# Kernel tuning notes

Hardware: AMD Instinct MI355X
Metric: run time of the kernel (lower is better)

The kernel has to match this reference:

```python
import jax, jax.numpy as jnp
import numpy as np

GROUPS = [21, 6, 17, 14, 20]
N = 78          # total nodes per graph
B = 8192        # batched graphs (original module processes one at a time)
RATIO = 0.2
LN_EPS = 1e-5


def _build_edges():
    """Replicates Graph_test mode='random' edge construction (incl. its offset quirk)."""
    rng = np.random.RandomState(0)
    edges = []
    offset = 0
    for num in GROUPS:
        for i in range(num):
            for j in range(num):
                if i != j:
                    edges.append((i + offset, j + offset))
        offset += num
    offset = 0
    for i in range(5):
        offset_2 = GROUPS[i]
        for j in range(i + 1, 5):
            for _i in range(GROUPS[i]):
                for _j in range(GROUPS[j]):
                    if _i + offset != _j + offset_2 and rng.random_sample() < RATIO:
                        edges.append((_i + offset, _j + offset_2))
            offset_2 += GROUPS[j]
        offset += GROUPS[i]
    return np.asarray(edges, dtype=np.int64).T  # [2, E]


def _ln(x, g, b):
    m = jnp.mean(x, axis=-1, keepdims=True)
    v = jnp.var(x, axis=-1, keepdims=True)
    return (x - m) * jax.lax.rsqrt(v + LN_EPS) * g + b


def _tconv(x, src, tgt, wq, bq, wk, bk, wv, bv, ws, bs, H, C):
    """PyG TransformerConv (concat=True, root_weight=True, no beta/edge_dim)."""
    n = x.shape[0]
    q = (x @ wq.T + bq).reshape(n, H, C)
    k = (x @ wk.T + bk).reshape(n, H, C)
    v = (x @ wv.T + bv).reshape(n, H, C)
    alpha = jnp.sum(q[tgt] * k[src], axis=-1) / np.sqrt(float(C))      # [E, H]
    amax = jax.ops.segment_max(alpha, tgt, num_segments=n)             # [N, H]
    e = jnp.exp(alpha - amax[tgt])
    den = jax.ops.segment_sum(e, tgt, num_segments=n)
    w = e / den[tgt]                                                   # softmax per target node
    out = jax.ops.segment_sum(w[..., None] * v[src], tgt, num_segments=n)
    return out.reshape(n, H * C) + (x @ ws.T + bs)                     # skip connection


def _forward(src, tgt, cli_data, radio_data, ln1_g, ln1_b, enc_w, enc_b,
             q1_w, q1_b, k1_w, k1_b, v1_w, v1_b, s1_w, s1_b,
             q2_w, q2_b, k2_w, k2_b, v2_w, v2_b, s2_w, s2_b,
             ln2_g, ln2_b, cls_w, cls_b):
    h = _ln(radio_data, ln1_g, ln1_b) @ enc_w.T + enc_b   # Linear(384,20)
    h = jax.nn.leaky_relu(h)                              # dropout = identity (eval)
    x = jnp.concatenate([cli_data, h], axis=1)[..., None]  # [B, 78, 1]

    def graph(xg):  # xg: [78, 1]
        y = jax.nn.leaky_relu(_tconv(xg, src, tgt, q1_w, q1_b, k1_w, k1_b,
                                     v1_w, v1_b, s1_w, s1_b, 4, 1))      # [78, 4]
        y = jax.nn.leaky_relu(_tconv(y, src, tgt, q2_w, q2_b, k2_w, k2_b,
                                     v2_w, v2_b, s2_w, s2_b, 1, 1))      # [78, 1]
        return y[:, 0]                                                    # [78]

    y = jax.vmap(graph)(x)                                # [B, 78]
    return _ln(y, ln2_g, ln2_b) @ cls_w.T + cls_b         # [B, 2]


def setup_inputs() -> dict:
    key = jax.random.key(0)
    ks = jax.random.split(key, 12)

    def xav(k, shape):
        lim = np.sqrt(6.0 / (shape[0] + shape[1]))
        return jax.random.uniform(k, shape, jnp.float32, -lim, lim)

    ei = jnp.asarray(_build_edges())
    return dict(
        cli_data=jax.random.normal(ks[0], (B, 58), jnp.float32),
        radio_data=jax.random.normal(ks[1], (B, 384), jnp.float32),
        edge_index=ei,
        ln1_g=jnp.ones((384,), jnp.float32), ln1_b=jnp.zeros((384,), jnp.float32),
        enc_w=xav(ks[2], (20, 384)), enc_b=jnp.zeros((20,), jnp.float32),
        q1_w=xav(ks[3], (4, 1)), q1_b=jnp.zeros((4,), jnp.float32),
        k1_w=xav(ks[4], (4, 1)), k1_b=jnp.zeros((4,), jnp.float32),
        v1_w=xav(ks[5], (4, 1)), v1_b=jnp.zeros((4,), jnp.float32),
        s1_w=xav(ks[6], (4, 1)), s1_b=jnp.zeros((4,), jnp.float32),
        q2_w=xav(ks[7], (1, 4)), q2_b=jnp.zeros((1,), jnp.float32),
        k2_w=xav(ks[8], (1, 4)), k2_b=jnp.zeros((1,), jnp.float32),
        v2_w=xav(ks[9], (1, 4)), v2_b=jnp.zeros((1,), jnp.float32),
        s2_w=xav(ks[10], (1, 4)), s2_b=jnp.zeros((1,), jnp.float32),
        ln2_g=jnp.ones((N,), jnp.float32), ln2_b=jnp.zeros((N,), jnp.float32),
        cls_w=xav(ks[11], (2, N)), cls_b=jnp.zeros((2,), jnp.float32),
    )


def reference(cli_data, radio_data, edge_index, ln1_g, ln1_b, enc_w, enc_b,
              q1_w, q1_b, k1_w, k1_b, v1_w, v1_b, s1_w, s1_b,
              q2_w, q2_b, k2_w, k2_b, v2_w, v2_b, s2_w, s2_b,
              ln2_g, ln2_b, cls_w, cls_b):
    src, tgt = edge_index[0], edge_index[1]
    return _forward(src, tgt, cli_data, radio_data, ln1_g, ln1_b, enc_w, enc_b,
                    q1_w, q1_b, k1_w, k1_b, v1_w, v1_b, s1_w, s1_b,
                    q2_w, q2_b, k2_w, k2_b, v2_w, v2_b, s2_w, s2_b,
                    ln2_g, ln2_b, cls_w, cls_b)


if __name__ == '__main__':
    out = reference(**setup_inputs())
    print(out.shape)
```

## Files before the change

kernel.cpp:

```cpp
#include <hip/hip_runtime.h>

#define LREL(x) ((x) > 0.0f ? (x) : 0.01f * (x))

constexpr int NNODE = 78;
constexpr int GPB   = 32;
constexpr int BLOCK = 512;
constexpr int ROWS  = 16;
constexpr int NI    = 5;
constexpr int PADS  = 33;

__global__ void build_csr_kernel(const int* __restrict__ ei, int E,
                                 int* __restrict__ row_ptr,
                                 int* __restrict__ csr_src) {
    __shared__ int cnt[NNODE];
    __shared__ int cur[NNODE];
    int tid = threadIdx.x;
    if (tid < NNODE) cnt[tid] = 0;
    __syncthreads();
    for (int e = tid; e < E; e += blockDim.x)
        atomicAdd(&cnt[ei[E + e]], 1);
    __syncthreads();
    if (tid == 0) {
        int acc = 0;
        for (int n = 0; n < NNODE; ++n) {
            row_ptr[n] = acc;
            cur[n]     = acc;
            acc += cnt[n];
        }
        row_ptr[NNODE] = acc;
    }
    __syncthreads();
    for (int e = tid; e < E; e += blockDim.x) {
        int t   = ei[E + e];
        int pos = atomicAdd(&cur[t], 1);
        csr_src[pos] = ei[e];
    }
}

__global__ __launch_bounds__(BLOCK, 2) void graph_fused_kernel(
    const float* __restrict__ cli,
    const float* __restrict__ radio,
    const float* __restrict__ ln1g, const float* __restrict__ ln1b,
    const float* __restrict__ encw, const float* __restrict__ encb,
    const float* __restrict__ q1w, const float* __restrict__ q1b,
    const float* __restrict__ k1w, const float* __restrict__ k1b,
    const float* __restrict__ v1w, const float* __restrict__ v1b,
    const float* __restrict__ s1w, const float* __restrict__ s1b,
    const float* __restrict__ q2w, const float* __restrict__ q2b,
    const float* __restrict__ k2w, const float* __restrict__ k2b,
    const float* __restrict__ v2w, const float* __restrict__ v2b,
    const float* __restrict__ s2w, const float* __restrict__ s2b,
    const float* __restrict__ ln2g, const float* __restrict__ ln2b,
    const float* __restrict__ clsw, const float* __restrict__ clsb,
    const int* __restrict__ row_ptr, const int* __restrict__ csr_src,
    int E, int Bn, float* __restrict__ out) {

    __shared__ float s_feat[NNODE * PADS];
    __shared__ float s_k2[NNODE * PADS];
    __shared__ float s_v2[NNODE * PADS];
    __shared__ float s_redA[ROWS * PADS];
    __shared__ float s_redB[ROWS * PADS];
    __shared__ float s_statM[PADS];
    __shared__ float s_statR[PADS];
    __shared__ int   s_rp[NNODE + 1];
    extern __shared__ int s_csr[];

    const int tid  = threadIdx.x;
    const int lane = tid & 63;
    const int w    = tid >> 6;
    const int half = (tid >> 5) & 1;
    const int l32  = tid & 31;
    const int b    = blockIdx.x;

    for (int i = tid; i < E; i += BLOCK) s_csr[i] = csr_src[i];
    if (tid == 0) s_csr[E] = 0;
    if (tid < NNODE + 1) s_rp[tid] = row_ptr[tid];

#pragma unroll
    for (int gg = 0; gg < 4; ++gg) {
        int g = w * 4 + gg;
        long gidx = (long)b * GPB + g;
        if (lane < 58 && gidx < Bn)
            s_feat[lane * PADS + g] = cli[gidx * 58 + lane];
    }

    const float4* radio4 = (const float4*)radio;
    const float4* encw4  = (const float4*)encw;
    const float4* g14    = (const float4*)ln1g;
    const float4* b14    = (const float4*)ln1b;
    float4 xn0[3], xn1[3];
    int gl0, gl1;
    {
#pragma unroll
        for (int pp = 0; pp < 2; ++pp) {
            int g = w * 4 + pp * 2 + half;
            long gidx = (long)b * GPB + g;
            bool ok = gidx < Bn;
            float4* xn = pp ? xn1 : xn0;
            if (pp) gl1 = g; else gl0 = g;
            float s = 0.0f, q = 0.0f;
#pragma unroll
            for (int i = 0; i < 3; ++i) {
                float4 v = ok ? radio4[gidx * 96 + l32 + 32 * i]
                              : make_float4(0, 0, 0, 0);
                xn[i] = v;
                s += v.x + v.y + v.z + v.w;
                q += v.x * v.x + v.y * v.y + v.z * v.z + v.w * v.w;
            }
#pragma unroll
            for (int o = 16; o; o >>= 1) {
                s += __shfl_xor(s, o, 32);
                q += __shfl_xor(q, o, 32);
            }
            float mean = s * (1.0f / 384.0f);
            float var  = q * (1.0f / 384.0f) - mean * mean;
            float rstd = rsqrtf(var + 1e-5f);
#pragma unroll
            for (int i = 0; i < 3; ++i) {
                float4 gv = g14[l32 + 32 * i];
                float4 bv = b14[l32 + 32 * i];
                float4 v  = xn[i];
                v.x = (v.x - mean) * rstd * gv.x + bv.x;
                v.y = (v.y - mean) * rstd * gv.y + bv.y;
                v.z = (v.z - mean) * rstd * gv.z + bv.z;
                v.w = (v.w - mean) * rstd * gv.w + bv.w;
                xn[i] = v;
            }
        }
        for (int j = 0; j < 20; ++j) {
            float4 w0 = encw4[j * 96 + l32];
            float4 w1 = encw4[j * 96 + l32 + 32];
            float4 w2 = encw4[j * 96 + l32 + 64];
#pragma unroll
            for (int pp = 0; pp < 2; ++pp) {
                const float4* xn = pp ? xn1 : xn0;
                float p = xn[0].x * w0.x;
                p = fmaf(xn[0].y, w0.y, p); p = fmaf(xn[0].z, w0.z, p);
                p = fmaf(xn[0].w, w0.w, p);
                p = fmaf(xn[1].x, w1.x, p); p = fmaf(xn[1].y, w1.y, p);
                p = fmaf(xn[1].z, w1.z, p); p = fmaf(xn[1].w, w1.w, p);
                p = fmaf(xn[2].x, w2.x, p); p = fmaf(xn[2].y, w2.y, p);
                p = fmaf(xn[2].z, w2.z, p); p = fmaf(xn[2].w, w2.w, p);
#pragma unroll
                for (int o = 16; o; o >>= 1) p += __shfl_xor(p, o, 32);
                if (l32 == j)
                    s_feat[(58 + j) * PADS + (pp ? gl1 : gl0)] =
                        LREL(p + encb[j]);
            }
        }
    }
    __syncthreads();

    const int g = tid & 31;
    const int r = tid >> 5;
    const long gbase = (long)b * GPB + g;
    const bool gok = gbase < Bn;

    const float Q1W0 = q1w[0], Q1W1 = q1w[1], Q1W2 = q1w[2], Q1W3 = q1w[3];
    const float Q1B0 = q1b[0], Q1B1 = q1b[1], Q1B2 = q1b[2], Q1B3 = q1b[3];
    const float K1W0 = k1w[0], K1W1 = k1w[1], K1W2 = k1w[2], K1W3 = k1w[3];
    const float K1B0 = k1b[0], K1B1 = k1b[1], K1B2 = k1b[2], K1B3 = k1b[3];
    const float V1W0 = v1w[0], V1W1 = v1w[1], V1W2 = v1w[2], V1W3 = v1w[3];
    const float V1B0 = v1b[0], V1B1 = v1b[1], V1B2 = v1b[2], V1B3 = v1b[3];
    const float S1W0 = s1w[0], S1W1 = s1w[1], S1W2 = s1w[2], S1W3 = s1w[3];
    const float S1B0 = s1b[0], S1B1 = s1b[1], S1B2 = s1b[2], S1B3 = s1b[3];
    const float Q2W0 = q2w[0], Q2W1 = q2w[1], Q2W2 = q2w[2], Q2W3 = q2w[3];
    const float K2W0 = k2w[0], K2W1 = k2w[1], K2W2 = k2w[2], K2W3 = k2w[3];
    const float V2W0 = v2w[0], V2W1 = v2w[1], V2W2 = v2w[2], V2W3 = v2w[3];
    const float S2W0 = s2w[0], S2W1 = s2w[1], S2W2 = s2w[2], S2W3 = s2w[3];
    const float Q2B = q2b[0], K2B = k2b[0], V2B = v2b[0], S2B = s2b[0];

    float y_q[NI], y_sk[NI];

#pragma unroll
    for (int k = 0; k < NI; ++k) {
        int n = r + ROWS * k;
        bool act = n < NNODE;
        int nn = act ? n : 0;
        float xv = s_feat[nn * PADS + g];
        float qh0 = fmaf(xv, Q1W0, Q1B0), qh1 = fmaf(xv, Q1W1, Q1B1);
        float qh2 = fmaf(xv, Q1W2, Q1B2), qh3 = fmaf(xv, Q1W3, Q1B3);
        float qa0 = qh0 * K1W0, cc0 = qh0 * K1B0;
        float qa1 = qh1 * K1W1, cc1 = qh1 * K1B1;
        float qa2 = qh2 * K1W2, cc2 = qh2 * K1B2;
        float qa3 = qh3 * K1W3, cc3 = qh3 * K1B3;
        float den0 = 0, den1 = 0, den2 = 0, den3 = 0;
        float wa0 = 0, wa1 = 0, wa2 = 0, wa3 = 0;
        int beg = s_rp[nn];
        int end = act ? s_rp[nn + 1] : beg;
        int i = beg;
        int sc = s_csr[i];
        while (i < end) {
            int sn = s_csr[i + 1];
            float t = s_feat[sc * PADS + g];
            float e0 = __expf(fmaf(qa0, t, cc0));
            float e1 = __expf(fmaf(qa1, t, cc1));
            float e2 = __expf(fmaf(qa2, t, cc2));
            float e3 = __expf(fmaf(qa3, t, cc3));
            den0 += e0; den1 += e1; den2 += e2; den3 += e3;
            wa0 = fmaf(e0, t, wa0); wa1 = fmaf(e1, t, wa1);
            wa2 = fmaf(e2, t, wa2); wa3 = fmaf(e3, t, wa3);
            sc = sn; ++i;
        }
        float y0 = LREL(fmaf(V1W0, wa0 / den0, V1B0) + fmaf(xv, S1W0, S1B0));
        float y1 = LREL(fmaf(V1W1, wa1 / den1, V1B1) + fmaf(xv, S1W1, S1B1));
        float y2 = LREL(fmaf(V1W2, wa2 / den2, V1B2) + fmaf(xv, S1W2, S1B2));
        float y3 = LREL(fmaf(V1W3, wa3 / den3, V1B3) + fmaf(xv, S1W3, S1B3));
        y_q[k]  = Q2B + y0 * Q2W0 + y1 * Q2W1 + y2 * Q2W2 + y3 * Q2W3;
        y_sk[k] = S2B + y0 * S2W0 + y1 * S2W1 + y2 * S2W2 + y3 * S2W3;
        float kk = K2B + y0 * K2W0 + y1 * K2W1 + y2 * K2W2 + y3 * K2W3;
        float vv = V2B + y0 * V2W0 + y1 * V2W1 + y2 * V2W2 + y3 * V2W3;
        if (act) {
            s_k2[n * PADS + g] = kk;
            s_v2[n * PADS + g] = vv;
        }
    }
    __syncthreads();

    float z[NI];
    float zs = 0, zq = 0;
#pragma unroll
    for (int k = 0; k < NI; ++k) {
        int n = r + ROWS * k;
        bool act = n < NNODE;
        int nn = act ? n : 0;
        float q = y_q[k];
        int beg = s_rp[nn];
        int end = act ? s_rp[nn + 1] : beg;
        float m = -1e30f;
        int i = beg;
        int sc = s_csr[i];
        while (i < end) {
            int sn = s_csr[i + 1];
            m = fmaxf(m, q * s_k2[sc * PADS + g]);
            sc = sn; ++i;
        }
        float den = 0, acc = 0;
        i = beg;
        sc = s_csr[i];
        while (i < end) {
            int sn = s_csr[i + 1];
            float kk = s_k2[sc * PADS + g];
            float vv = s_v2[sc * PADS + g];
            float e = __expf(fmaf(q, kk, -m));
            den += e;
            acc = fmaf(e, vv, acc);
            sc = sn; ++i;
        }
        float zz = LREL(acc / den + y_sk[k]);
        z[k] = zz;
        if (act) { zs += zz; zq = fmaf(zz, zz, zq); }
    }

    s_redA[r * PADS + g] = zs;
    s_redB[r * PADS + g] = zq;
    __syncthreads();
    if (r == 0) {
        float a = 0, bb = 0;
#pragma unroll
        for (int i = 0; i < ROWS; ++i) {
            a  += s_redA[i * PADS + g];
            bb += s_redB[i * PADS + g];
        }
        float mean = a * (1.0f / 78.0f);
        float var  = bb * (1.0f / 78.0f) - mean * mean;
        s_statM[g] = mean;
        s_statR[g] = rsqrtf(var + 1e-5f);
    }
    __syncthreads();
    float mean = s_statM[g], rstd = s_statR[g];
    float p0 = 0, p1 = 0;
#pragma unroll
    for (int k = 0; k < NI; ++k) {
        int n = r + ROWS * k;
        if (n < NNODE) {
            float zn = fmaf((z[k] - mean) * rstd, ln2g[n], ln2b[n]);
            p0 = fmaf(zn, clsw[n], p0);
            p1 = fmaf(zn, clsw[NNODE + n], p1);
        }
    }
    __syncthreads();
    s_redA[r * PADS + g] = p0;
    s_redB[r * PADS + g] = p1;
    __syncthreads();
    if (r == 0 && gok) {
        float a = 0, bb = 0;
#pragma unroll
        for (int i = 0; i < ROWS; ++i) {
            a  += s_redA[i * PADS + g];
            bb += s_redB[i * PADS + g];
        }
        out[gbase * 2 + 0] = a + clsb[0];
        out[gbase * 2 + 1] = bb + clsb[1];
    }
}

extern "C" void kernel_launch(void* const* d_in, const int* in_sizes, int n_in,
                              void* d_out, int out_size, void* d_ws, size_t ws_size,
                              hipStream_t stream) {
    const float* cli   = (const float*)d_in[0];
    const float* radio = (const float*)d_in[1];
    const int*   ei    = (const int*)d_in[2];
    const float* ln1g = (const float*)d_in[3];
    const float* ln1b = (const float*)d_in[4];
    const float* encw = (const float*)d_in[5];
    const float* encb = (const float*)d_in[6];
    const float* q1w  = (const float*)d_in[7];
    const float* q1b  = (const float*)d_in[8];
    const float* k1w  = (const float*)d_in[9];
    const float* k1b  = (const float*)d_in[10];
    const float* v1w  = (const float*)d_in[11];
    const float* v1b  = (const float*)d_in[12];
    const float* s1w  = (const float*)d_in[13];
    const float* s1b  = (const float*)d_in[14];
    const float* q2w  = (const float*)d_in[15];
    const float* q2b  = (const float*)d_in[16];
    const float* k2w  = (const float*)d_in[17];
    const float* k2b  = (const float*)d_in[18];
    const float* v2w  = (const float*)d_in[19];
    const float* v2b  = (const float*)d_in[20];
    const float* s2w  = (const float*)d_in[21];
    const float* s2b  = (const float*)d_in[22];
    const float* ln2g = (const float*)d_in[23];
    const float* ln2b = (const float*)d_in[24];
    const float* clsw = (const float*)d_in[25];
    const float* clsb = (const float*)d_in[26];

    const int E  = in_sizes[2] / 2;
    const int Bn = in_sizes[0] / 58;

    int* row_ptr = (int*)d_ws;
    int* csr_src = row_ptr + 80;

    build_csr_kernel<<<1, 256, 0, stream>>>(ei, E, row_ptr, csr_src);

    const int grid = (Bn + GPB - 1) / GPB;
    size_t shmem = (size_t)(E + 1) * sizeof(int);
    graph_fused_kernel<<<grid, BLOCK, shmem, stream>>>(
        cli, radio, ln1g, ln1b, encw, encb,
        q1w, q1b, k1w, k1b, v1w, v1b, s1w, s1b,
        q2w, q2b, k2w, k2b, v2w, v2b, s2w, s2b,
        ln2g, ln2b, clsw, clsb,
        row_ptr, csr_src, E, Bn, (float*)d_out);
}
```

Baseline: 171.5 us.

## Split encoder into separate kernel and load-balance graph conv by node degree

Moves the LayerNorm+Linear encoder into its own kernel that writes a 20-wide hidden buffer to workspace. The graph conv kernel now handles 16 graphs per block with 32 row-threads, and assigns nodes to rows via a degree-sorted permutation so work per thread is more even. It also pre-scales CSR indices by the pad stride, folds log2e into the weights to use exp2f, drops the constant key-bias term in layer-1 softmax, unrolls the edge loops by two, and replaces shared-memory reductions with wavefront shuffles. In exchange it adds a global round trip for the hidden features and one extra kernel launch.

```diff
diff --git a/kernel.cpp b/kernel.cpp
--- a/kernel.cpp
+++ b/kernel.cpp
@@ -1,24 +1,29 @@
 #include <hip/hip_runtime.h>
 
 #define LREL(x) ((x) > 0.0f ? (x) : 0.01f * (x))
+#define LOG2E 1.44269504f
 
 constexpr int NNODE = 78;
-constexpr int GPB   = 32;
-constexpr int BLOCK = 512;
-constexpr int ROWS  = 16;
-constexpr int NI    = 5;
-constexpr int PADS  = 33;
+constexpr int GPB   = 16;
+constexpr int ROWS  = 32;
+constexpr int BLOCK = GPB * ROWS;
+constexpr int NI    = 3;
+constexpr int PADS  = 17;
 
 __global__ void build_csr_kernel(const int* __restrict__ ei, int E,
                                  int* __restrict__ row_ptr,
-                                 int* __restrict__ csr_src) {
+                                 int* __restrict__ csr_src,
+                                 int* __restrict__ perm) {
     __shared__ int cnt[NNODE];
     __shared__ int cur[NNODE];
+    __shared__ int deg[NNODE];
     int tid = threadIdx.x;
     if (tid < NNODE) cnt[tid] = 0;
     __syncthreads();
     for (int e = tid; e < E; e += blockDim.x)
         atomicAdd(&cnt[ei[E + e]], 1);
+    __syncthreads();
+    if (tid < NNODE) deg[tid] = cnt[tid];
     __syncthreads();
     if (tid == 0) {
         int acc = 0;
@@ -29,19 +34,108 @@
         }
         row_ptr[NNODE] = acc;
     }
+    if (tid < NNODE) {
+        int d = deg[tid], rank = 0;
+        for (int m = 0; m < NNODE; ++m) {
+            int dm = deg[m];
+            rank += (dm > d) || (dm == d && m < tid);
+        }
+        perm[rank] = tid;
+    }
+    if (tid >= NNODE && tid < ROWS * NI) perm[tid] = -1;
     __syncthreads();
     for (int e = tid; e < E; e += blockDim.x) {
         int t   = ei[E + e];
         int pos = atomicAdd(&cur[t], 1);
-        csr_src[pos] = ei[e];
+        csr_src[pos] = ei[e] * PADS;
     }
 }
 
-__global__ __launch_bounds__(BLOCK, 2) void graph_fused_kernel(
-    const float* __restrict__ cli,
+__global__ __launch_bounds__(256) void encode_kernel(
     const float* __restrict__ radio,
     const float* __restrict__ ln1g, const float* __restrict__ ln1b,
     const float* __restrict__ encw, const float* __restrict__ encb,
+    int Bn, float* __restrict__ hout) {
+
+    const int tid  = threadIdx.x;
+    const int w    = tid >> 6;
+    const int half = (tid >> 5) & 1;
+    const int l32  = tid & 31;
+
+    const float4* radio4 = (const float4*)radio;
+    const float4* encw4  = (const float4*)encw;
+    const float4* g14    = (const float4*)ln1g;
+    const float4* b14    = (const float4*)ln1b;
+
+    float4 xn0[3], xn1[3];
+    const long g0 = (long)blockIdx.x * 16 + w * 4 + half;
+    const long g1 = g0 + 2;
+
+#pragma unroll
+    for (int pp = 0; pp < 2; ++pp) {
+        long gidx = pp ? g1 : g0;
+        bool ok = gidx < Bn;
+        float4* xn = pp ? xn1 : xn0;
+        float s = 0.0f, q = 0.0f;
+#pragma unroll
+        for (int i = 0; i < 3; ++i) {
+            float4 v = ok ? radio4[gidx * 96 + l32 + 32 * i]
+                          : make_float4(0, 0, 0, 0);
+            xn[i] = v;
+            s += v.x + v.y + v.z + v.w;
+            q += v.x * v.x + v.y * v.y + v.z * v.z + v.w * v.w;
+        }
+#pragma unroll
+        for (int o = 16; o; o >>= 1) {
+            s += __shfl_xor(s, o, 32);
+            q += __shfl_xor(q, o, 32);
+        }
+        float mean = s * (1.0f / 384.0f);
+        float var  = q * (1.0f / 384.0f) - mean * mean;
+        float rstd = rsqrtf(var + 1e-5f);
+#pragma unroll
+        for (int i = 0; i < 3; ++i) {
+            float4 gv = g14[l32 + 32 * i];
+            float4 bv = b14[l32 + 32 * i];
+            float4 v  = xn[i];
+            v.x = (v.x - mean) * rstd * gv.x + bv.x;
+            v.y = (v.y - mean) * rstd * gv.y + bv.y;
+            v.z = (v.z - mean) * rstd * gv.z + bv.z;
+            v.w = (v.w - mean) * rstd * gv.w + bv.w;
+            xn[i] = v;
+        }
+    }
+
+    float h0 = 0.0f, h1 = 0.0f;
+    for (int j = 0; j < 20; ++j) {
+        float4 w0 = encw4[j * 96 + l32];
+        float4 w1 = encw4[j * 96 + l32 + 32];
+        float4 w2 = encw4[j * 96 + l32 + 64];
+#pragma unroll
+        for (int pp = 0; pp < 2; ++pp) {
+            const float4* xn = pp ? xn1 : xn0;
+            float p = xn[0].x * w0.x;
+            p = fmaf(xn[0].y, w0.y, p); p = fmaf(xn[0].z, w0.z, p);
+            p = fmaf(xn[0].w, w0.w, p);
+            p = fmaf(xn[1].x, w1.x, p); p = fmaf(xn[1].y, w1.y, p);
+            p = fmaf(xn[1].z, w1.z, p); p = fmaf(xn[1].w, w1.w, p);
+            p = fmaf(xn[2].x, w2.x, p); p = fmaf(xn[2].y, w2.y, p);
+            p = fmaf(xn[2].w, w2.w, p); p = fmaf(xn[2].z, w2.z, p);
+#pragma unroll
+            for (int o = 16; o; o >>= 1) p += __shfl_xor(p, o, 32);
+            if (pp) h1 = (l32 == j) ? p : h1;
+            else    h0 = (l32 == j) ? p : h0;
+        }
+    }
+    if (l32 < 20) {
+        float eb = encb[l32];
+        if (g0 < Bn) hout[g0 * 20 + l32] = LREL(h0 + eb);
+        if (g1 < Bn) hout[g1 * 20 + l32] = LREL(h1 + eb);
+    }
+}
+
+__global__ __launch_bounds__(BLOCK, 4) void graph_conv_kernel(
+    const float* __restrict__ cli, const float* __restrict__ hin,
     const float* __restrict__ q1w, const float* __restrict__ q1b,
     const float* __restrict__ k1w, const float* __restrict__ k1b,
     const float* __restrict__ v1w, const float* __restrict__ v1b,
@@ -53,113 +147,43 @@
     const float* __restrict__ ln2g, const float* __restrict__ ln2b,
     const float* __restrict__ clsw, const float* __restrict__ clsb,
     const int* __restrict__ row_ptr, const int* __restrict__ csr_src,
+    const int* __restrict__ perm,
     int E, int Bn, float* __restrict__ out) {
 
     __shared__ float s_feat[NNODE * PADS];
     __shared__ float s_k2[NNODE * PADS];
     __shared__ float s_v2[NNODE * PADS];
-    __shared__ float s_redA[ROWS * PADS];
-    __shared__ float s_redB[ROWS * PADS];
-    __shared__ float s_statM[PADS];
-    __shared__ float s_statR[PADS];
+    __shared__ float s_redA[8 * PADS];
+    __shared__ float s_redB[8 * PADS];
+    __shared__ float s_statM[GPB];
+    __shared__ float s_statR[GPB];
     __shared__ int   s_rp[NNODE + 1];
+    __shared__ int   s_slot[ROWS * NI];
     extern __shared__ int s_csr[];
 
     const int tid  = threadIdx.x;
+    const int g    = tid & 15;
+    const int r    = tid >> 4;
+    const int w    = tid >> 6;
     const int lane = tid & 63;
-    const int w    = tid >> 6;
-    const int half = (tid >> 5) & 1;
-    const int l32  = tid & 31;
-    const int b    = blockIdx.x;
+    const long base = (long)blockIdx.x * GPB;
 
     for (int i = tid; i < E; i += BLOCK) s_csr[i] = csr_src[i];
-    if (tid == 0) s_csr[E] = 0;
     if (tid < NNODE + 1) s_rp[tid] = row_ptr[tid];
-
-#pragma unroll
-    for (int gg = 0; gg < 4; ++gg) {
-        int g = w * 4 + gg;
-        long gidx = (long)b * GPB + g;
-        if (lane < 58 && gidx < Bn)
-            s_feat[lane * PADS + g] = cli[gidx * 58 + lane];
-    }
-
-    const float4* radio4 = (const float4*)radio;
-    const float4* encw4  = (const float4*)encw;
-    const float4* g14    = (const float4*)ln1g;
-    const float4* b14    = (const float4*)ln1b;
-    float4 xn0[3], xn1[3];
-    int gl0, gl1;
-    {
-#pragma unroll
-        for (int pp = 0; pp < 2; ++pp) {
-            int g = w * 4 + pp * 2 + half;
-            long gidx = (long)b * GPB + g;
-            bool ok = gidx < Bn;
-            float4* xn = pp ? xn1 : xn0;
-            if (pp) gl1 = g; else gl0 = g;
-            float s = 0.0f, q = 0.0f;
-#pragma unroll
-            for (int i = 0; i < 3; ++i) {
-                float4 v = ok ? radio4[gidx * 96 + l32 + 32 * i]
-                              : make_float4(0, 0, 0, 0);
-                xn[i] = v;
-                s += v.x + v.y + v.z + v.w;
-                q += v.x * v.x + v.y * v.y + v.z * v.z + v.w * v.w;
-            }
-#pragma unroll
-            for (int o = 16; o; o >>= 1) {
-                s += __shfl_xor(s, o, 32);
-                q += __shfl_xor(q, o, 32);
-            }
-            float mean = s * (1.0f / 384.0f);
-            float var  = q * (1.0f / 384.0f) - mean * mean;
-            float rstd = rsqrtf(var + 1e-5f);
-#pragma unroll
-            for (int i = 0; i < 3; ++i) {
-                float4 gv = g14[l32 + 32 * i];
-                float4 bv = b14[l32 + 32 * i];
-                float4 v  = xn[i];
-                v.x = (v.x - mean) * rstd * gv.x + bv.x;
-                v.y = (v.y - mean) * rstd * gv.y + bv.y;
-                v.z = (v.z - mean) * rstd * gv.z + bv.z;
-                v.w = (v.w - mean) * rstd * gv.w + bv.w;
-                xn[i] = v;
-            }
-        }
-        for (int j = 0; j < 20; ++j) {
-            float4 w0 = encw4[j * 96 + l32];
-            float4 w1 = encw4[j * 96 + l32 + 32];
-            float4 w2 = encw4[j * 96 + l32 + 64];
-#pragma unroll
-            for (int pp = 0; pp < 2; ++pp) {
-                const float4* xn = pp ? xn1 : xn0;
-                float p = xn[0].x * w0.x;
-                p = fmaf(xn[0].y, w0.y, p); p = fmaf(xn[0].z, w0.z, p);
-                p = fmaf(xn[0].w, w0.w, p);
-                p = fmaf(xn[1].x, w1.x, p); p = fmaf(xn[1].y, w1.y, p);
-                p = fmaf(xn[1].z, w1.z, p); p = fmaf(xn[1].w, w1.w, p);
-                p = fmaf(xn[2].x, w2.x, p); p = fmaf(xn[2].y, w2.y, p);
-                p = fmaf(xn[2].z, w2.z, p); p = fmaf(xn[2].w, w2.w, p);
-#pragma unroll
-                for (int o = 16; o; o >>= 1) p += __shfl_xor(p, o, 32);
-                if (l32 == j)
-                    s_feat[(58 + j) * PADS + (pp ? gl1 : gl0)] =
-                        LREL(p + encb[j]);
-            }
-        }
-    }
-    __syncthreads();
-
-    const int g = tid & 31;
-    const int r = tid >> 5;
-    const long gbase = (long)b * GPB + g;
-    const bool gok = gbase < Bn;
+    if (tid < ROWS * NI) s_slot[tid] = perm[tid];
+    for (int idx = tid; idx < GPB * 58; idx += BLOCK) {
+        int gg = idx / 58, c = idx - gg * 58;
+        if (base + gg < Bn) s_feat[c * PADS + gg] = cli[(base + gg) * 58 + c];
+    }
+    if (tid < GPB * 20) {
+        int gg = tid / 20, j = tid - gg * 20;
+        if (base + gg < Bn) s_feat[(58 + j) * PADS + gg] = hin[(base + gg) * 20 + j];
+    }
 
     const float Q1W0 = q1w[0], Q1W1 = q1w[1], Q1W2 = q1w[2], Q1W3 = q1w[3];
     const float Q1B0 = q1b[0], Q1B1 = q1b[1], Q1B2 = q1b[2], Q1B3 = q1b[3];
-    const float K1W0 = k1w[0], K1W1 = k1w[1], K1W2 = k1w[2], K1W3 = k1w[3];
-    const float K1B0 = k1b[0], K1B1 = k1b[1], K1B2 = k1b[2], K1B3 = k1b[3];
+    const float K1L0 = k1w[0] * LOG2E, K1L1 = k1w[1] * LOG2E;
+    const float K1L2 = k1w[2] * LOG2E, K1L3 = k1w[3] * LOG2E;
     const float V1W0 = v1w[0], V1W1 = v1w[1], V1W2 = v1w[2], V1W3 = v1w[3];
     const float V1B0 = v1b[0], V1B1 = v1b[1], V1B2 = v1b[2], V1B3 = v1b[3];
     const float S1W0 = s1w[0], S1W1 = s1w[1], S1W2 = s1w[2], S1W3 = s1w[3];
@@ -169,38 +193,50 @@
     const float V2W0 = v2w[0], V2W1 = v2w[1], V2W2 = v2w[2], V2W3 = v2w[3];
     const float S2W0 = s2w[0], S2W1 = s2w[1], S2W2 = s2w[2], S2W3 = s2w[3];
     const float Q2B = q2b[0], K2B = k2b[0], V2B = v2b[0], S2B = s2b[0];
-
-    float y_q[NI], y_sk[NI];
+    __syncthreads();
+
+    int   nodes[NI];
+    float y_q[NI], y_sk[NI], z[NI];
 
 #pragma unroll
     for (int k = 0; k < NI; ++k) {
-        int n = r + ROWS * k;
-        bool act = n < NNODE;
+        int n = s_slot[k * ROWS + r];
+        nodes[k] = n;
+        bool act = n >= 0;
         int nn = act ? n : 0;
         float xv = s_feat[nn * PADS + g];
         float qh0 = fmaf(xv, Q1W0, Q1B0), qh1 = fmaf(xv, Q1W1, Q1B1);
         float qh2 = fmaf(xv, Q1W2, Q1B2), qh3 = fmaf(xv, Q1W3, Q1B3);
-        float qa0 = qh0 * K1W0, cc0 = qh0 * K1B0;
-        float qa1 = qh1 * K1W1, cc1 = qh1 * K1B1;
-        float qa2 = qh2 * K1W2, cc2 = qh2 * K1B2;
-        float qa3 = qh3 * K1W3, cc3 = qh3 * K1B3;
+        float qa0 = qh0 * K1L0, qa1 = qh1 * K1L1;
+        float qa2 = qh2 * K1L2, qa3 = qh3 * K1L3;
         float den0 = 0, den1 = 0, den2 = 0, den3 = 0;
         float wa0 = 0, wa1 = 0, wa2 = 0, wa3 = 0;
         int beg = s_rp[nn];
         int end = act ? s_rp[nn + 1] : beg;
         int i = beg;
-        int sc = s_csr[i];
-        while (i < end) {
-            int sn = s_csr[i + 1];
-            float t = s_feat[sc * PADS + g];
-            float e0 = __expf(fmaf(qa0, t, cc0));
-            float e1 = __expf(fmaf(qa1, t, cc1));
-            float e2 = __expf(fmaf(qa2, t, cc2));
-            float e3 = __expf(fmaf(qa3, t, cc3));
-            den0 += e0; den1 += e1; den2 += e2; den3 += e3;
-            wa0 = fmaf(e0, t, wa0); wa1 = fmaf(e1, t, wa1);
-            wa2 = fmaf(e2, t, wa2); wa3 = fmaf(e3, t, wa3);
-            sc = sn; ++i;
+        for (; i + 1 < end; i += 2) {
+            int c0 = s_csr[i], c1 = s_csr[i + 1];
+            float t0 = s_feat[c0 + g];
+            float t1 = s_feat[c1 + g];
+            float ea0 = exp2f(qa0 * t0), eb0 = exp2f(qa0 * t1);
+            float ea1 = exp2f(qa1 * t0), eb1 = exp2f(qa1 * t1);
+            float ea2 = exp2f(qa2 * t0), eb2 = exp2f(qa2 * t1);
+            float ea3 = exp2f(qa3 * t0), eb3 = exp2f(qa3 * t1);
+            den0 += ea0 + eb0; den1 += ea1 + eb1;
+            den2 += ea2 + eb2; den3 += ea3 + eb3;
+            wa0 = fmaf(ea0, t0, fmaf(eb0, t1, wa0));
+            wa1 = fmaf(ea1, t0, fmaf(eb1, t1, wa1));
+            wa2 = fmaf(ea2, t0, fmaf(eb2, t1, wa2));
+            wa3 = fmaf(ea3, t0, fmaf(eb3, t1, wa3));
+        }
+        if (i < end) {
+            int c0 = s_csr[i];
+            float t0 = s_feat[c0 + g];
+            float ea0 = exp2f(qa0 * t0), ea1 = exp2f(qa1 * t0);
+            float ea2 = exp2f(qa2 * t0), ea3 = exp2f(qa3 * t0);
+            den0 += ea0; den1 += ea1; den2 += ea2; den3 += ea3;
+            wa0 = fmaf(ea0, t0, wa0); wa1 = fmaf(ea1, t0, wa1);
+            wa2 = fmaf(ea2, t0, wa2); wa3 = fmaf(ea3, t0, wa3);
         }
         float y0 = LREL(fmaf(V1W0, wa0 / den0, V1B0) + fmaf(xv, S1W0, S1B0));
         float y1 = LREL(fmaf(V1W1, wa1 / den1, V1B1) + fmaf(xv, S1W1, S1B1));
@@ -208,90 +244,98 @@
         float y3 = LREL(fmaf(V1W3, wa3 / den3, V1B3) + fmaf(xv, S1W3, S1B3));
         y_q[k]  = Q2B + y0 * Q2W0 + y1 * Q2W1 + y2 * Q2W2 + y3 * Q2W3;
         y_sk[k] = S2B + y0 * S2W0 + y1 * S2W1 + y2 * S2W2 + y3 * S2W3;
-        float kk = K2B + y0 * K2W0 + y1 * K2W1 + y2 * K2W2 + y3 * K2W3;
-        float vv = V2B + y0 * V2W0 + y1 * V2W1 + y2 * V2W2 + y3 * V2W3;
         if (act) {
-            s_k2[n * PADS + g] = kk;
-            s_v2[n * PADS + g] = vv;
-        }
-    }
-    __syncthreads();
-
-    float z[NI];
+            s_k2[n * PADS + g] = K2B + y0 * K2W0 + y1 * K2W1 + y2 * K2W2 + y3 * K2W3;
+            s_v2[n * PADS + g] = V2B + y0 * V2W0 + y1 * V2W1 + y2 * V2W2 + y3 * V2W3;
+        }
+    }
+    __syncthreads();
+
     float zs = 0, zq = 0;
 #pragma unroll
     for (int k = 0; k < NI; ++k) {
-        int n = r + ROWS * k;
-        bool act = n < NNODE;
+        int n = nodes[k];
+        bool act = n >= 0;
         int nn = act ? n : 0;
         float q = y_q[k];
         int beg = s_rp[nn];
         int end = act ? s_rp[nn + 1] : beg;
         float m = -1e30f;
+        for (int i = beg; i < end; ++i)
+            m = fmaxf(m, q * s_k2[s_csr[i] + g]);
+        float ql = q * LOG2E, ml = m * LOG2E;
+        float den = 0, acc = 0;
         int i = beg;
-        int sc = s_csr[i];
-        while (i < end) {
-            int sn = s_csr[i + 1];
-            m = fmaxf(m, q * s_k2[sc * PADS + g]);
-            sc = sn; ++i;
-        }
-        float den = 0, acc = 0;
-        i = beg;
-        sc = s_csr[i];
-        while (i < end) {
-            int sn = s_csr[i + 1];
-            float kk = s_k2[sc * PADS + g];
-            float vv = s_v2[sc * PADS + g];
-            float e = __expf(fmaf(q, kk, -m));
-            den += e;
-            acc = fmaf(e, vv, acc);
-            sc = sn; ++i;
+        for (; i + 1 < end; i += 2) {
+            int c0 = s_csr[i], c1 = s_csr[i + 1];
+            float k0 = s_k2[c0 + g], k1v = s_k2[c1 + g];
+            float v0 = s_v2[c0 + g], v1v = s_v2[c1 + g];
+            float e0 = exp2f(fmaf(ql, k0, -ml));
+            float e1 = exp2f(fmaf(ql, k1v, -ml));
+            den += e0 + e1;
+            acc = fmaf(e0, v0, fmaf(e1, v1v, acc));
+        }
+        if (i < end) {
+            int c0 = s_csr[i];
+            float e0 = exp2f(fmaf(ql, s_k2[c0 + g], -ml));
+            den += e0;
+            acc = fmaf(e0, s_v2[c0 + g], acc);
         }
         float zz = LREL(acc / den + y_sk[k]);
         z[k] = zz;
         if (act) { zs += zz; zq = fmaf(zz, zz, zq); }
     }
 
-    s_redA[r * PADS + g] = zs;
-    s_redB[r * PADS + g] = zq;
-    __syncthreads();
-    if (r == 0) {
+    zs += __shfl_xor(zs, 16, 64); zs += __shfl_xor(zs, 32, 64);
+    zq += __shfl_xor(zq, 16, 64); zq += __shfl_xor(zq, 32, 64);
+    if (lane < 16) {
+        s_redA[w * PADS + lane] = zs;
+        s_redB[w * PADS + lane] = zq;
+    }
+    __syncthreads();
+    if (tid < GPB) {
         float a = 0, bb = 0;
 #pragma unroll
-        for (int i = 0; i < ROWS; ++i) {
-            a  += s_redA[i * PADS + g];
-            bb += s_redB[i * PADS + g];
+        for (int i = 0; i < 8; ++i) {
+            a  += s_redA[i * PADS + tid];
+            bb += s_redB[i * PADS + tid];
         }
         float mean = a * (1.0f / 78.0f);
         float var  = bb * (1.0f / 78.0f) - mean * mean;
-        s_statM[g] = mean;
-        s_statR[g] = rsqrtf(var + 1e-5f);
+        s_statM[tid] = mean;
+        s_statR[tid] = rsqrtf(var + 1e-5f);
     }
     __syncthreads();
     float mean = s_statM[g], rstd = s_statR[g];
     float p0 = 0, p1 = 0;
 #pragma unroll
     for (int k = 0; k < NI; ++k) {
-        int n = r + ROWS * k;
-        if (n < NNODE) {
+        int n = nodes[k];
+        if (n >= 0) {
             float zn = fmaf((z[k] - mean) * rstd, ln2g[n], ln2b[n]);
             p0 = fmaf(zn, clsw[n], p0);
             p1 = fmaf(zn, clsw[NNODE + n], p1);
         }
     }
-    __syncthreads();
-    s_redA[r * PADS + g] = p0;
-    s_redB[r * PADS + g] = p1;
-    __syncthreads();
-    if (r == 0 && gok) {
+    p0 += __shfl_xor(p0, 16, 64); p0 += __shfl_xor(p0, 32, 64);
+    p1 += __shfl_xor(p1, 16, 64); p1 += __shfl_xor(p1, 32, 64);
+    if (lane < 16) {
+        s_redA[w * PADS + lane] = p0;
+        s_redB[w * PADS + lane] = p1;
+    }
+    __syncthreads();
+    if (tid < GPB) {
         float a = 0, bb = 0;
 #pragma unroll
-        for (int i = 0; i < ROWS; ++i) {
-            a  += s_redA[i * PADS + g];
-            bb += s_redB[i * PADS + g];
-        }
-        out[gbase * 2 + 0] = a + clsb[0];
-        out[gbase * 2 + 1] = bb + clsb[1];
+        for (int i = 0; i < 8; ++i) {
+            a  += s_redA[i * PADS + tid];
+            bb += s_redB[i * PADS + tid];
+        }
+        long gi = base + tid;
+        if (gi < Bn) {
+            out[gi * 2 + 0] = a + clsb[0];
+            out[gi * 2 + 1] = bb + clsb[1];
+        }
     }
 }
 
@@ -331,15 +375,21 @@
 
     int* row_ptr = (int*)d_ws;
     int* csr_src = row_ptr + 80;
-
-    build_csr_kernel<<<1, 256, 0, stream>>>(ei, E, row_ptr, csr_src);
+    int* perm    = csr_src + E;
+    int  off     = (80 + E + ROWS * NI + 7) & ~7;
+    float* h     = (float*)((int*)d_ws + off);
+
+    build_csr_kernel<<<1, 256, 0, stream>>>(ei, E, row_ptr, csr_src, perm);
+
+    const int egrid = (Bn + 15) / 16;
+    encode_kernel<<<egrid, 256, 0, stream>>>(radio, ln1g, ln1b, encw, encb, Bn, h);
 
     const int grid = (Bn + GPB - 1) / GPB;
-    size_t shmem = (size_t)(E + 1) * sizeof(int);
-    graph_fused_kernel<<<grid, BLOCK, shmem, stream>>>(
-        cli, radio, ln1g, ln1b, encw, encb,
+    size_t shmem = (size_t)E * sizeof(int);
+    graph_conv_kernel<<<grid, BLOCK, shmem, stream>>>(
+        cli, h,
         q1w, q1b, k1w, k1b, v1w, v1b, s1w, s1b,
         q2w, q2b, k2w, k2b, v2w, v2b, s2w, s2b,
         ln2g, ln2b, clsw, clsb,
-        row_ptr, csr_src, E, Bn, (float*)d_out);
+        row_ptr, csr_src, perm, E, Bn, (float*)d_out);
 }
```

Result: faster. 165.2 us (-3.7%).
